# Kernel tuning notes

Measured on AMD Instinct MI355X. Metric: run time of the kernel, lower is better.

## Reference

```python
import jax, jax.numpy as jnp
import numpy as np

WINDOW_SIZE = 11
DATA_RANGE = 1.0
CHANNELS = 3


def _gaussian_window(window_size=WINDOW_SIZE, channel=CHANNELS):
    # 1D gaussian with sigma=1.0, normalized, then outer product -> 2D window
    x = np.arange(window_size)
    g = np.exp(-(x - window_size // 2) ** 2 / (2.0 * 1.0 ** 2))
    g = g / g.sum()
    w2d = np.outer(g, g)  # [K, K]
    # depthwise kernel in OIHW: [C, 1, K, K]
    w = np.broadcast_to(w2d, (channel, 1, window_size, window_size)).copy()
    return jnp.asarray(w, dtype=jnp.float32)


def _depthwise_conv(x, window):
    pad = WINDOW_SIZE // 2
    return jax.lax.conv_general_dilated(
        x, window,
        window_strides=(1, 1),
        padding=[(pad, pad), (pad, pad)],
        feature_group_count=CHANNELS,
        dimension_numbers=("NCHW", "OIHW", "NCHW"),
    )


def setup_inputs() -> dict:
    key = jax.random.key(0)
    k1, k2 = jax.random.split(key)
    pred = jax.random.uniform(k1, (16, 3, 512, 512), dtype=jnp.float32)
    target = jax.random.uniform(k2, (16, 3, 512, 512), dtype=jnp.float32)
    return {"pred": pred, "target": target}


def reference(pred, target):
    window = _gaussian_window()
    mu_x = _depthwise_conv(pred, window)
    mu_y = _depthwise_conv(target, window)
    sigma_x = _depthwise_conv(pred * pred, window) - mu_x * mu_x
    sigma_y = _depthwise_conv(target * target, window) - mu_y * mu_y
    sigma_xy = _depthwise_conv(pred * target, window) - mu_x * mu_y
    C1 = (0.01 * DATA_RANGE) ** 2
    C2 = (0.03 * DATA_RANGE) ** 2
    # NOTE: faithful to source, which (non-standardly) squares the variances in the denominator
    ssim_map = (2 * mu_x * mu_y + C1) * (2 * sigma_xy + C2) / (
        (mu_x * mu_x + mu_y * mu_y + C1) * (sigma_x * sigma_x + sigma_y * sigma_y + C2)
    )
    return ssim_map.mean()
```

## Files before the change

kernel.cpp:

```cpp
#include <hip/hip_runtime.h>
#include <stdint.h>


#define HH 512
#define WW 512
#define PLANES 48
#define TW 64
#define TH 16
#define RR 5
#define KK 11
#define IN_H (TH + 2 * RR)
#define HALO_W 74
#define SW 84
#define COFF 3
#define RBW 76
#define NBLOCKS (PLANES * (WW / TW) * (HH / TH))
#define NTHREADS 256
#define NSTAGE (IN_H * 20)
#define NITEMS1 (HALO_W * 4)
#define TOTAL_ELEMS (PLANES * HH * WW)

typedef _Float16 half2v __attribute__((ext_vector_type(2)));
typedef float float2v __attribute__((ext_vector_type(2)));

constexpr float G_[KK] = {
    1.4867195147342977e-06f, 1.3383022576488537e-04f, 4.4318484119380075e-03f,
    5.3990966513188063e-02f, 2.4197072451914337e-01f, 3.9894228040143270e-01f,
    2.4197072451914337e-01f, 5.3990966513188063e-02f, 4.4318484119380075e-03f,
    1.3383022576488537e-04f, 1.4867195147342977e-06f};

__device__ __forceinline__ half2v u2h(uint32_t u) {
  return __builtin_bit_cast(half2v, u);
}
__device__ __forceinline__ uint32_t packrtn(float a, float b) {
  half2v h = {(_Float16)a, (_Float16)b};
  return __builtin_bit_cast(uint32_t, h);
}

__global__ __launch_bounds__(NTHREADS, 4) void ssim_tile_kernel(
    const float* __restrict__ pred, const float* __restrict__ targ,
    float* __restrict__ partial) {
  __shared__ __align__(16) float sp[IN_H][SW];
  __shared__ __align__(16) float st[IN_H][SW];
  __shared__ __align__(16) uint2 rbAB[TH][RBW];
  __shared__ __align__(16) float rbC[TH][RBW];
  __shared__ float wsums[4];

  const int tid = threadIdx.x;
  const int bid = blockIdx.x;
  const int plane = bid >> 8;
  const int tile = bid & 255;
  const int x0 = (tile & 7) * TW;
  const int y0 = (tile >> 3) * TH;
  const float* pp = pred + (size_t)plane * (HH * WW);
  const float* tp = targ + (size_t)plane * (HH * WW);

  for (int i = tid; i < NSTAGE; i += NTHREADS) {
    const int r = i / 20;
    const int cg = i - r * 20;
    const int gy = y0 + r - RR;
    const int gx = x0 - 8 + cg * 4;
    float4 pv = make_float4(0.f, 0.f, 0.f, 0.f);
    float4 tv = pv;
    if (gy >= 0 && gy < HH && gx >= 0 && gx <= WW - 4) {
      const int o = gy * WW + gx;
      pv = *reinterpret_cast<const float4*>(pp + o);
      tv = *reinterpret_cast<const float4*>(tp + o);
    }
    *reinterpret_cast<float4*>(&sp[r][cg * 4]) = pv;
    *reinterpret_cast<float4*>(&st[r][cg * 4]) = tv;
  }
  __syncthreads();

  for (int i = tid; i < NITEMS1; i += NTHREADS) {
    const int c = i % HALO_W;
    const int rg = i / HALO_W;
    const int yb = rg * 4;
    const int sc = c + COFF;

    float pv[14], tv[14];
#pragma unroll
    for (int m = 0; m < 14; ++m) {
      pv[m] = sp[yb + m][sc];
      tv[m] = st[yb + m][sc];
    }

    float2v s01[4] = {{0,0},{0,0},{0,0},{0,0}};
    float2v s23[4] = {{0,0},{0,0},{0,0},{0,0}};
    float s4[4] = {0,0,0,0};
#pragma unroll
    for (int q = 0; q < 14; ++q) {
      const float a = pv[q];
      const float b = tv[q];
      const float2v av = {a, b};
      const float2v sq = av * av;
      const float ab = a * b;
#pragma unroll
      for (int j = 0; j < 4; ++j) {
        if (q < j || q > j + 10) continue;
        const float w = G_[q - j];
        const float2v w2 = {w, w};
        s01[j] = __builtin_elementwise_fma(w2, av, s01[j]);
        s23[j] = __builtin_elementwise_fma(w2, sq, s23[j]);
        s4[j] = fmaf(w, ab, s4[j]);
      }
    }

#pragma unroll
    for (int j = 0; j < 4; ++j) {
      uint2 u;
      u.x = packrtn(s01[j].x, s01[j].y);
      u.y = packrtn(s23[j].x, s23[j].y);
      rbAB[yb + j][c] = u;
      rbC[yb + j][c] = s4[j];
    }
  }
  __syncthreads();

  float lsum = 0.f;
  {
    const int m = tid & 15;
    const int y = tid >> 4;
    const int cb = m << 2;

    uint2 qv[14];
#pragma unroll
    for (int h = 0; h < 7; ++h) {
      uint4 w = *reinterpret_cast<const uint4*>(&rbAB[y][cb + 2 * h]);
      qv[2*h]   = make_uint2(w.x, w.y);
      qv[2*h+1] = make_uint2(w.z, w.w);
    }
    float cv[16];
#pragma unroll
    for (int h = 0; h < 4; ++h) {
      *reinterpret_cast<float4*>(&cv[4*h]) =
          *reinterpret_cast<const float4*>(&rbC[y][cb + 4 * h]);
    }

    float2v fa[14], fb[14];
#pragma unroll
    for (int k = 0; k < 14; ++k) {
      half2v ha = u2h(qv[k].x), hb = u2h(qv[k].y);
      fa[k] = float2v{(float)ha.x, (float)ha.y};
      fb[k] = float2v{(float)hb.x, (float)hb.y};
    }

    float2v accA[4], accB[4];
    float sC[4];
#pragma unroll
    for (int j = 0; j < 4; ++j) {
      float2v a = {0, 0}, b = {0, 0};
      float c = 0.f;
#pragma unroll
      for (int k = 0; k < KK; ++k) {
        const float2v w2 = {G_[k], G_[k]};
        a = __builtin_elementwise_fma(w2, fa[j + k], a);
        b = __builtin_elementwise_fma(w2, fb[j + k], b);
        c = fmaf(G_[k], cv[j + k], c);
      }
      accA[j] = a; accB[j] = b; sC[j] = c;
    }

    const float C1 = 1.0e-4f;
    const float C2 = 9.0e-4f;
#pragma unroll
    for (int j = 0; j < 4; ++j) {
      const float mu_x = accA[j].x;
      const float mu_y = accA[j].y;
      const float2v sv = __builtin_elementwise_fma(-accA[j], accA[j], accB[j]);
      const float sxy = sC[j] - mu_x * mu_y;
      const float num = (2.f * mu_x * mu_y + C1) * (2.f * sxy + C2);
      const float den = (mu_x * mu_x + mu_y * mu_y + C1) *
                        (fmaf(sv.x, sv.x, fmaf(sv.y, sv.y, C2)));
      lsum = fmaf(num, __builtin_amdgcn_rcpf(den), lsum);
    }
  }

#pragma unroll
  for (int off = 32; off > 0; off >>= 1) lsum += __shfl_xor(lsum, off, 64);
  if ((tid & 63) == 0) wsums[tid >> 6] = lsum;
  __syncthreads();
  if (tid == 0)
    partial[bid] = (wsums[0] + wsums[1]) + (wsums[2] + wsums[3]);
}

__global__ __launch_bounds__(1024) void ssim_reduce_kernel(
    const float* __restrict__ partial, float* __restrict__ out) {
  float s = 0.f;
  for (int i = threadIdx.x; i < NBLOCKS; i += 1024) s += partial[i];
#pragma unroll
  for (int off = 32; off > 0; off >>= 1) s += __shfl_xor(s, off, 64);
  __shared__ float ws[16];
  if ((threadIdx.x & 63) == 0) ws[threadIdx.x >> 6] = s;
  __syncthreads();
  if (threadIdx.x == 0) {
    float t = 0.f;
#pragma unroll
    for (int i = 0; i < 16; ++i) t += ws[i];
    out[0] = t * (1.0f / (float)TOTAL_ELEMS);
  }
}

extern "C" void kernel_launch(void* const* d_in, const int* in_sizes, int n_in,
                              void* d_out, int out_size, void* d_ws,
                              size_t ws_size, hipStream_t stream) {
  const float* pred = (const float*)d_in[0];
  const float* targ = (const float*)d_in[1];
  float* out = (float*)d_out;
  float* partial = (float*)d_ws;

  ssim_tile_kernel<<<NBLOCKS, NTHREADS, 0, stream>>>(pred, targ, partial);
  ssim_reduce_kernel<<<1, 1024, 0, stream>>>(partial, out);
}
```

Before: 69.93 us.

## Truncate Gaussian taps to nine and add fast interior staging path

The two outermost Gaussian taps (weight about 1.5e-6) are dropped in both the vertical and horizontal passes, so fewer shared-memory loads and FMAs run per output. A separate staging loop for interior tiles skips the per-element bounds checks. Dropping taps changes the result slightly, which is an approximation of the reference convolution.

```diff
diff --git a/kernel.cpp b/kernel.cpp
--- a/kernel.cpp
+++ b/kernel.cpp
@@ -8,7 +8,6 @@
 #define TW 64
 #define TH 16
 #define RR 5
-#define KK 11
 #define IN_H (TH + 2 * RR)
 #define HALO_W 74
 #define SW 84
@@ -23,7 +22,7 @@
 typedef _Float16 half2v __attribute__((ext_vector_type(2)));
 typedef float float2v __attribute__((ext_vector_type(2)));
 
-constexpr float G_[KK] = {
+constexpr float G_[11] = {
     1.4867195147342977e-06f, 1.3383022576488537e-04f, 4.4318484119380075e-03f,
     5.3990966513188063e-02f, 2.4197072451914337e-01f, 3.9894228040143270e-01f,
     2.4197072451914337e-01f, 5.3990966513188063e-02f, 4.4318484119380075e-03f,
@@ -55,20 +54,32 @@
   const float* pp = pred + (size_t)plane * (HH * WW);
   const float* tp = targ + (size_t)plane * (HH * WW);
 
-  for (int i = tid; i < NSTAGE; i += NTHREADS) {
-    const int r = i / 20;
-    const int cg = i - r * 20;
-    const int gy = y0 + r - RR;
-    const int gx = x0 - 8 + cg * 4;
-    float4 pv = make_float4(0.f, 0.f, 0.f, 0.f);
-    float4 tv = pv;
-    if (gy >= 0 && gy < HH && gx >= 0 && gx <= WW - 4) {
-      const int o = gy * WW + gx;
-      pv = *reinterpret_cast<const float4*>(pp + o);
-      tv = *reinterpret_cast<const float4*>(tp + o);
-    }
-    *reinterpret_cast<float4*>(&sp[r][cg * 4]) = pv;
-    *reinterpret_cast<float4*>(&st[r][cg * 4]) = tv;
+  if ((x0 >= 64) && (x0 <= 384) && (y0 >= 16) && (y0 <= 480)) {
+    for (int i = tid; i < NSTAGE; i += NTHREADS) {
+      const int r = i / 20;
+      const int cg = i - r * 20;
+      const int o = (y0 + r - RR) * WW + (x0 - 8 + cg * 4);
+      *reinterpret_cast<float4*>(&sp[r][cg * 4]) =
+          *reinterpret_cast<const float4*>(pp + o);
+      *reinterpret_cast<float4*>(&st[r][cg * 4]) =
+          *reinterpret_cast<const float4*>(tp + o);
+    }
+  } else {
+    for (int i = tid; i < NSTAGE; i += NTHREADS) {
+      const int r = i / 20;
+      const int cg = i - r * 20;
+      const int gy = y0 + r - RR;
+      const int gx = x0 - 8 + cg * 4;
+      float4 pv = make_float4(0.f, 0.f, 0.f, 0.f);
+      float4 tv = pv;
+      if (gy >= 0 && gy < HH && gx >= 0 && gx <= WW - 4) {
+        const int o = gy * WW + gx;
+        pv = *reinterpret_cast<const float4*>(pp + o);
+        tv = *reinterpret_cast<const float4*>(tp + o);
+      }
+      *reinterpret_cast<float4*>(&sp[r][cg * 4]) = pv;
+      *reinterpret_cast<float4*>(&st[r][cg * 4]) = tv;
+    }
   }
   __syncthreads();
 
@@ -78,26 +89,26 @@
     const int yb = rg * 4;
     const int sc = c + COFF;
 
-    float pv[14], tv[14];
-#pragma unroll
-    for (int m = 0; m < 14; ++m) {
-      pv[m] = sp[yb + m][sc];
-      tv[m] = st[yb + m][sc];
+    float pv[12], tv[12];
+#pragma unroll
+    for (int m = 0; m < 12; ++m) {
+      pv[m] = sp[yb + 1 + m][sc];
+      tv[m] = st[yb + 1 + m][sc];
     }
 
     float2v s01[4] = {{0,0},{0,0},{0,0},{0,0}};
     float2v s23[4] = {{0,0},{0,0},{0,0},{0,0}};
     float s4[4] = {0,0,0,0};
 #pragma unroll
-    for (int q = 0; q < 14; ++q) {
-      const float a = pv[q];
-      const float b = tv[q];
+    for (int q = 1; q <= 12; ++q) {
+      const float a = pv[q - 1];
+      const float b = tv[q - 1];
       const float2v av = {a, b};
       const float2v sq = av * av;
       const float ab = a * b;
 #pragma unroll
       for (int j = 0; j < 4; ++j) {
-        if (q < j || q > j + 10) continue;
+        if (j < q - 9 || j > q - 1) continue;
         const float w = G_[q - j];
         const float2v w2 = {w, w};
         s01[j] = __builtin_elementwise_fma(w2, av, s01[j]);
@@ -137,10 +148,10 @@
           *reinterpret_cast<const float4*>(&rbC[y][cb + 4 * h]);
     }
 
-    float2v fa[14], fb[14];
-#pragma unroll
-    for (int k = 0; k < 14; ++k) {
-      half2v ha = u2h(qv[k].x), hb = u2h(qv[k].y);
+    float2v fa[12], fb[12];
+#pragma unroll
+    for (int k = 0; k < 12; ++k) {
+      half2v ha = u2h(qv[k + 1].x), hb = u2h(qv[k + 1].y);
       fa[k] = float2v{(float)ha.x, (float)ha.y};
       fb[k] = float2v{(float)hb.x, (float)hb.y};
     }
@@ -152,11 +163,12 @@
       float2v a = {0, 0}, b = {0, 0};
       float c = 0.f;
 #pragma unroll
-      for (int k = 0; k < KK; ++k) {
-        const float2v w2 = {G_[k], G_[k]};
+      for (int k = 0; k < 9; ++k) {
+        const float w = G_[k + 1];
+        const float2v w2 = {w, w};
         a = __builtin_elementwise_fma(w2, fa[j + k], a);
         b = __builtin_elementwise_fma(w2, fb[j + k], b);
-        c = fmaf(G_[k], cv[j + k], c);
+        c = fmaf(w, cv[j + 1 + k], c);
       }
       accA[j] = a; accB[j] = b; sC[j] = c;
     }
```

After: 73.85 us. 1.06x slower.

## Stage input tile transposed in LDS for vectorized vertical-pass reads

Applied to the files above, without the earlier changes.

Input tiles are now staged into shared memory column-major (column by row, padded to 28), so the vertical pass reads its 14 needed rows with four float4 LDS loads instead of 14 scalar loads per array. Global loads become scalar per-row gathers (four rows per thread), and a fast path skips bounds checks for interior tiles. The trade is fewer, wider LDS reads in the compute stage against less-vectorized global loads and possible bank conflicts on the transposed float4 stores.

```diff
diff --git a/kernel.cpp b/kernel.cpp
--- a/kernel.cpp
+++ b/kernel.cpp
@@ -9,14 +9,12 @@
 #define TH 16
 #define RR 5
 #define KK 11
-#define IN_H (TH + 2 * RR)
 #define HALO_W 74
-#define SW 84
-#define COFF 3
+#define TRP 28
 #define RBW 76
 #define NBLOCKS (PLANES * (WW / TW) * (HH / TH))
 #define NTHREADS 256
-#define NSTAGE (IN_H * 20)
+#define NSTAGE (HALO_W * 7)
 #define NITEMS1 (HALO_W * 4)
 #define TOTAL_ELEMS (PLANES * HH * WW)
 
@@ -40,8 +38,8 @@
 __global__ __launch_bounds__(NTHREADS, 4) void ssim_tile_kernel(
     const float* __restrict__ pred, const float* __restrict__ targ,
     float* __restrict__ partial) {
-  __shared__ __align__(16) float sp[IN_H][SW];
-  __shared__ __align__(16) float st[IN_H][SW];
+  __shared__ __align__(16) float spT[HALO_W][TRP];
+  __shared__ __align__(16) float stT[HALO_W][TRP];
   __shared__ __align__(16) uint2 rbAB[TH][RBW];
   __shared__ __align__(16) float rbC[TH][RBW];
   __shared__ float wsums[4];
@@ -55,20 +53,41 @@
   const float* pp = pred + (size_t)plane * (HH * WW);
   const float* tp = targ + (size_t)plane * (HH * WW);
 
-  for (int i = tid; i < NSTAGE; i += NTHREADS) {
-    const int r = i / 20;
-    const int cg = i - r * 20;
-    const int gy = y0 + r - RR;
-    const int gx = x0 - 8 + cg * 4;
-    float4 pv = make_float4(0.f, 0.f, 0.f, 0.f);
-    float4 tv = pv;
-    if (gy >= 0 && gy < HH && gx >= 0 && gx <= WW - 4) {
-      const int o = gy * WW + gx;
-      pv = *reinterpret_cast<const float4*>(pp + o);
-      tv = *reinterpret_cast<const float4*>(tp + o);
-    }
-    *reinterpret_cast<float4*>(&sp[r][cg * 4]) = pv;
-    *reinterpret_cast<float4*>(&st[r][cg * 4]) = tv;
+  const bool interior = (x0 >= 64) && (x0 <= 384) && (y0 >= 16) && (y0 <= 480);
+
+  if (interior) {
+    for (int i = tid; i < NSTAGE; i += NTHREADS) {
+      const int c = i % HALO_W;
+      const int rg = i / HALO_W;
+      const float* pb = pp + (y0 - RR + 4 * rg) * WW + (x0 - RR + c);
+      const float* tb = tp + (y0 - RR + 4 * rg) * WW + (x0 - RR + c);
+      float4 pv, tv;
+      pv.x = pb[0]; pv.y = pb[WW]; pv.z = pb[2 * WW]; pv.w = pb[3 * WW];
+      tv.x = tb[0]; tv.y = tb[WW]; tv.z = tb[2 * WW]; tv.w = tb[3 * WW];
+      *reinterpret_cast<float4*>(&spT[c][4 * rg]) = pv;
+      *reinterpret_cast<float4*>(&stT[c][4 * rg]) = tv;
+    }
+  } else {
+    for (int i = tid; i < NSTAGE; i += NTHREADS) {
+      const int c = i % HALO_W;
+      const int rg = i / HALO_W;
+      const int gx = x0 - RR + c;
+      const bool xok = (gx >= 0) && (gx < WW);
+      float4 pv = make_float4(0.f, 0.f, 0.f, 0.f);
+      float4 tv = pv;
+      if (xok) {
+#pragma unroll
+        for (int w = 0; w < 4; ++w) {
+          const int gy = y0 - RR + 4 * rg + w;
+          if (gy >= 0 && gy < HH) {
+            reinterpret_cast<float*>(&pv)[w] = pp[gy * WW + gx];
+            reinterpret_cast<float*>(&tv)[w] = tp[gy * WW + gx];
+          }
+        }
+      }
+      *reinterpret_cast<float4*>(&spT[c][4 * rg]) = pv;
+      *reinterpret_cast<float4*>(&stT[c][4 * rg]) = tv;
+    }
   }
   __syncthreads();
 
@@ -76,13 +95,14 @@
     const int c = i % HALO_W;
     const int rg = i / HALO_W;
     const int yb = rg * 4;
-    const int sc = c + COFF;
-
-    float pv[14], tv[14];
-#pragma unroll
-    for (int m = 0; m < 14; ++m) {
-      pv[m] = sp[yb + m][sc];
-      tv[m] = st[yb + m][sc];
+
+    float pv[16], tv[16];
+#pragma unroll
+    for (int h = 0; h < 4; ++h) {
+      *reinterpret_cast<float4*>(&pv[4 * h]) =
+          *reinterpret_cast<const float4*>(&spT[c][yb + 4 * h]);
+      *reinterpret_cast<float4*>(&tv[4 * h]) =
+          *reinterpret_cast<const float4*>(&stT[c][yb + 4 * h]);
     }
 
     float2v s01[4] = {{0,0},{0,0},{0,0},{0,0}};
```

After: 66.12 us. -5.4%, faster.
